# Optimization experiments

Measured on AMD Instinct MI355X. Metric: run time of the kernel, lower is better.

Reference implementation:

```python
import jax, jax.numpy as jnp
import numpy as np

B, NQ, NK, D = 64, 1024, 1024, 128
MASK_VALUE = -1e6


def setup_inputs() -> dict:
    key = jax.random.key(0)
    kq, kk, kv, kl = jax.random.split(key, 4)
    queries = jax.random.normal(kq, (B, NQ, D), dtype=jnp.float32)
    keys = jax.random.normal(kk, (B, NK, D), dtype=jnp.float32)
    values = jax.random.normal(kv, (B, NK, D), dtype=jnp.float32)
    valid_lens = jax.random.randint(kl, (B,), 1, NK + 1, dtype=jnp.int32)
    return {"queries": queries, "keys": keys, "values": values, "valid_lens": valid_lens}


def reference(queries, keys, values, valid_lens):
    d = queries.shape[-1]
    # scores: [B, Nq, Nk]
    scores = jnp.einsum("bqd,bkd->bqk", queries, keys) / jnp.sqrt(jnp.float32(d))
    # valid_lens [B] -> mask over last (key) axis, same for every query row
    key_pos = jnp.arange(scores.shape[-1])  # [Nk]
    mask = key_pos[None, None, :] < valid_lens[:, None, None]  # [B,1,Nk] broadcast
    scores = jnp.where(mask, scores, jnp.float32(MASK_VALUE))
    attn = jax.nn.softmax(scores, axis=-1)
    # dropout p=0.0 (eval): identity
    return jnp.einsum("bqk,bkd->bqd", attn, values)
```

## Files before the change

kernel.cpp:

```cpp
#include <hip/hip_runtime.h>

typedef __bf16 bf16x8 __attribute__((ext_vector_type(8)));
typedef __bf16 bf16x2 __attribute__((ext_vector_type(2)));
typedef float f32x4 __attribute__((ext_vector_type(4)));
typedef float f32x16 __attribute__((ext_vector_type(16)));
typedef int i32x4 __attribute__((ext_vector_type(4)));

namespace {
constexpr int kNQ = 1024;
constexpr int kNK = 1024;
constexpr int kD = 128;
constexpr int kBK = 32;
constexpr int kTileElems = 4096;
constexpr float kScaleLog2e = 0.12751742f;
}

__device__ __forceinline__ int packbf(float a, float b) {
    bf16x2 t; t[0] = (__bf16)a; t[1] = (__bf16)b;
    return __builtin_bit_cast(int, t);
}

__global__ void repack(const float* __restrict__ K, const float* __restrict__ V,
                       const int* __restrict__ VL,
                       __bf16* __restrict__ Kimg, __bf16* __restrict__ Vimg,
                       int* __restrict__ perm) {
    const int blk = blockIdx.x;

    if (blk == 64 * 32) {
        const int t = threadIdx.x;
        if (t < 64) {
            const int v = VL[t];
            int rank = 0;
            for (int j = 0; j < 64; ++j) {
                const int vj = VL[j];
                rank += (vj > v) || (vj == v && j < t);
            }
            perm[rank] = t;
        }
        return;
    }

    const int b = blk >> 5, t = blk & 31;
    if (t * kBK >= VL[b]) return;
    const int tid = threadIdx.x;
    __shared__ float vbuf[32 * 132];

    const size_t tileofs = (size_t)(b * 32 + t) * kTileElems;

    {
        const int key = tid >> 3, s = tid & 7;
        const float* src = K + (((size_t)b * kNK + t * kBK + key) * kD + s * 16);
        const f32x4 x0 = *(const f32x4*)(src + 0);
        const f32x4 x1 = *(const f32x4*)(src + 4);
        const f32x4 x2 = *(const f32x4*)(src + 8);
        const f32x4 x3 = *(const f32x4*)(src + 12);
        bf16x8 h0, h1;
        #pragma unroll
        for (int j = 0; j < 4; ++j) {
            h0[j] = (__bf16)x0[j]; h0[4 + j] = (__bf16)x1[j];
            h1[j] = (__bf16)x2[j]; h1[4 + j] = (__bf16)x3[j];
        }
        *(bf16x8*)(Kimg + tileofs + (s * 64 + key) * 8)      = h0;
        *(bf16x8*)(Kimg + tileofs + (s * 64 + 32 + key) * 8) = h1;
    }

    {
        const int r = tid >> 3, col0 = (tid & 7) * 16;
        const float* src = V + (((size_t)b * kNK + t * kBK + r) * kD + col0);
        #pragma unroll
        for (int j = 0; j < 4; ++j) {
            const f32x4 x = *(const f32x4*)(src + j * 4);
            *(f32x4*)&vbuf[r * 132 + col0 + j * 4] = x;
        }
    }
    __syncthreads();
    #pragma unroll
    for (int it = 0; it < 2; ++it) {
        const int ch  = tid + it * 256;
        const int db  = ch >> 7;
        const int s   = (ch >> 6) & 1;
        const int hi  = (ch >> 5) & 1;
        const int key = ch & 31;
        const int d   = db * 32 + key;
        const int k8  = s * 16 + hi * 8;
        bf16x8 h;
        #pragma unroll
        for (int j = 0; j < 8; ++j) h[j] = (__bf16)vbuf[(k8 + j) * 132 + d];
        *(bf16x8*)(Vimg + tileofs + ch * 8) = h;
    }
}

__global__ __launch_bounds__(256, 2)
void fa_fwd(const float* __restrict__ Q, const int* __restrict__ VL,
            const int* __restrict__ perm, const __bf16* __restrict__ Kimg,
            const __bf16* __restrict__ Vimg, float* __restrict__ O)
{
    const int tid  = threadIdx.x;
    const int wave = tid >> 6;
    const int lane = tid & 63;
    const int key  = lane & 31;
    const int hi   = lane >> 5;

    const int i = blockIdx.x;
    const int j = i & 255;
    const int rank = (i >> 8) ? (511 - j) : j;

    const int b  = perm[rank >> 3];
    const int q0 = (rank & 7) * 128 + wave * 32;

    const int valid  = VL[b];
    const int ntiles = (valid + kBK - 1) / kBK;
    const __bf16* kbase = Kimg + (size_t)b * 32 * kTileElems;
    const __bf16* vbase = Vimg + (size_t)b * 32 * kTileElems;
    const int fofs = lane * 8;

    bf16x8 qf[8];
    {
        const float* qp = Q + ((size_t)b * kNQ + q0 + key) * kD + hi * 8;
        #pragma unroll
        for (int s = 0; s < 8; ++s) {
            const f32x4 x0 = *(const f32x4*)(qp + s * 16);
            const f32x4 x1 = *(const f32x4*)(qp + s * 16 + 4);
            #pragma unroll
            for (int jj = 0; jj < 4; ++jj) {
                qf[s][jj]     = (__bf16)x0[jj];
                qf[s][4 + jj] = (__bf16)x1[jj];
            }
        }
    }

    bf16x8 kr[8], vr[8];
    #pragma unroll
    for (int s = 0; s < 8; ++s)
        kr[s] = *(const bf16x8*)(kbase + s * 512 + fofs);
    #pragma unroll
    for (int f = 0; f < 8; ++f)
        vr[f] = *(const bf16x8*)(vbase + f * 512 + fofs);

    f32x16 acc0, acc1, acc2, acc3;
    #pragma unroll
    for (int r = 0; r < 16; ++r) { acc0[r]=0.f; acc1[r]=0.f; acc2[r]=0.f; acc3[r]=0.f; }
    float lsum = 0.f;

    const int xaddr = (lane ^ 32) << 2;
    const int hi4   = hi << 2;

    for (int t = 0; t < ntiles; ++t) {
        f32x16 sa, sb;
        #pragma unroll
        for (int r = 0; r < 16; ++r) { sa[r] = 0.f; sb[r] = 0.f; }
        __builtin_amdgcn_s_setprio(1);
        #pragma unroll
        for (int s = 0; s < 4; ++s)
            sa = __builtin_amdgcn_mfma_f32_32x32x16_bf16(kr[s], qf[s], sa, 0, 0, 0);
        #pragma unroll
        for (int s = 4; s < 8; ++s)
            sb = __builtin_amdgcn_mfma_f32_32x32x16_bf16(kr[s], qf[s], sb, 0, 0, 0);
        __builtin_amdgcn_s_setprio(0);

        if (t + 1 < ntiles) {
            const __bf16* kt = kbase + (size_t)(t + 1) * kTileElems;
            #pragma unroll
            for (int s = 0; s < 8; ++s)
                kr[s] = *(const bf16x8*)(kt + s * 512 + fofs);
        }

        f32x16 sv = sa + sb;

        const int kb = t * kBK;
        if (kb + kBK > valid) {
            #pragma unroll
            for (int r = 0; r < 16; ++r) {
                const int cr = (r & 3) + 8 * (r >> 2);
                if (kb + cr + hi4 >= valid) sv[r] = -1e30f;
            }
        }

        #pragma unroll
        for (int r = 0; r < 16; ++r) sv[r] = __builtin_amdgcn_exp2f(sv[r] * kScaleLog2e);

        {
            float a0 = sv[0]+sv[1], a1 = sv[2]+sv[3], a2 = sv[4]+sv[5], a3 = sv[6]+sv[7];
            float a4 = sv[8]+sv[9], a5 = sv[10]+sv[11], a6 = sv[12]+sv[13], a7 = sv[14]+sv[15];
            lsum += ((a0+a1)+(a2+a3)) + ((a4+a5)+(a6+a7));
        }

        int w[8], pw[8];
        #pragma unroll
        for (int jp = 0; jp < 8; ++jp) w[jp] = packbf(sv[2*jp], sv[2*jp+1]);
        #pragma unroll
        for (int jp = 0; jp < 8; ++jp) pw[jp] = __builtin_amdgcn_ds_bpermute(xaddr, w[jp]);

        i32x4 f0, f1;
        f0[0] = hi ? pw[2] : w[0];
        f0[1] = hi ? pw[3] : w[1];
        f0[2] = hi ? w[2]  : pw[0];
        f0[3] = hi ? w[3]  : pw[1];
        f1[0] = hi ? pw[6] : w[4];
        f1[1] = hi ? pw[7] : w[5];
        f1[2] = hi ? w[6]  : pw[4];
        f1[3] = hi ? w[7]  : pw[5];
        const bf16x8 pfs0 = __builtin_bit_cast(bf16x8, f0);
        const bf16x8 pfs1 = __builtin_bit_cast(bf16x8, f1);

        __builtin_amdgcn_s_setprio(1);
        acc0 = __builtin_amdgcn_mfma_f32_32x32x16_bf16(pfs0, vr[0], acc0, 0, 0, 0);
        acc1 = __builtin_amdgcn_mfma_f32_32x32x16_bf16(pfs0, vr[2], acc1, 0, 0, 0);
        acc2 = __builtin_amdgcn_mfma_f32_32x32x16_bf16(pfs0, vr[4], acc2, 0, 0, 0);
        acc3 = __builtin_amdgcn_mfma_f32_32x32x16_bf16(pfs0, vr[6], acc3, 0, 0, 0);
        acc0 = __builtin_amdgcn_mfma_f32_32x32x16_bf16(pfs1, vr[1], acc0, 0, 0, 0);
        acc1 = __builtin_amdgcn_mfma_f32_32x32x16_bf16(pfs1, vr[3], acc1, 0, 0, 0);
        acc2 = __builtin_amdgcn_mfma_f32_32x32x16_bf16(pfs1, vr[5], acc2, 0, 0, 0);
        acc3 = __builtin_amdgcn_mfma_f32_32x32x16_bf16(pfs1, vr[7], acc3, 0, 0, 0);
        __builtin_amdgcn_s_setprio(0);

        if (t + 1 < ntiles) {
            const __bf16* vt = vbase + (size_t)(t + 1) * kTileElems;
            #pragma unroll
            for (int f = 0; f < 8; ++f)
                vr[f] = *(const bf16x8*)(vt + f * 512 + fofs);
        }
    }

    const int plb = __builtin_amdgcn_ds_bpermute(xaddr, __builtin_bit_cast(int, lsum));
    const float linv = 1.0f / (lsum + __builtin_bit_cast(float, plb));
    float* ob = O + ((size_t)b * kNQ + q0) * kD;
    const int hib = hi << 4;
    #pragma unroll
    for (int r = 0; r < 16; ++r) {
        const int cr = (r & 3) + 8 * (r >> 2);
        const int iv = __builtin_amdgcn_ds_bpermute((cr << 2) + hib,
                                                    __builtin_bit_cast(int, linv));
        const float inv = __builtin_bit_cast(float, iv);
        const int q = cr + hi4;
        ob[q * kD +   0 + key] = acc0[r] * inv;
        ob[q * kD +  32 + key] = acc1[r] * inv;
        ob[q * kD +  64 + key] = acc2[r] * inv;
        ob[q * kD +  96 + key] = acc3[r] * inv;
    }
}

extern "C" void kernel_launch(void* const* d_in, const int* in_sizes, int n_in,
                              void* d_out, int out_size, void* d_ws, size_t ws_size,
                              hipStream_t stream) {
    const float* Q = (const float*)d_in[0];
    const float* K = (const float*)d_in[1];
    const float* V = (const float*)d_in[2];
    const int*  VL = (const int*)d_in[3];
    float* O = (float*)d_out;

    int* perm = (int*)d_ws;
    __bf16* Kimg = (__bf16*)((char*)d_ws + 4096);
    __bf16* Vimg = (__bf16*)((char*)d_ws + 4096 + (size_t)16 * 1024 * 1024);

    repack<<<dim3(64 * 32 + 1), 256, 0, stream>>>(K, V, VL, Kimg, Vimg, perm);
    fa_fwd<<<dim3(512), 256, 0, stream>>>(Q, VL, perm, Kimg, Vimg, O);
}
```

Baseline: 163.5 us.

## Split key range across two blocks and add combine kernel

Each query chunk is now processed by two blocks that each cover half of the key tiles, doubling the grid. Partial unnormalized outputs and row sums are written to global memory, and a new combine kernel adds the halves and divides by the total sum. This aims to increase parallelism and balance per-block work, at the cost of extra global traffic for the partial outputs and an additional kernel launch.

```diff
diff --git a/kernel.cpp b/kernel.cpp
--- a/kernel.cpp
+++ b/kernel.cpp
@@ -10,6 +10,7 @@
 constexpr int kNQ = 1024;
 constexpr int kNK = 1024;
 constexpr int kD = 128;
+constexpr int kB  = 64;
 constexpr int kBK = 32;
 constexpr int kTileElems = 4096;
 constexpr float kScaleLog2e = 0.12751742f;
@@ -93,7 +94,8 @@
 __global__ __launch_bounds__(256, 2)
 void fa_fwd(const float* __restrict__ Q, const int* __restrict__ VL,
             const int* __restrict__ perm, const __bf16* __restrict__ Kimg,
-            const __bf16* __restrict__ Vimg, float* __restrict__ O)
+            const __bf16* __restrict__ Vimg, float* __restrict__ Onum,
+            float* __restrict__ Npart, float* __restrict__ Lpart)
 {
     const int tid  = threadIdx.x;
     const int wave = tid >> 6;
@@ -102,14 +104,21 @@
     const int hi   = lane >> 5;
 
     const int i = blockIdx.x;
-    const int j = i & 255;
-    const int rank = (i >> 8) ? (511 - j) : j;
-
-    const int b  = perm[rank >> 3];
-    const int q0 = (rank & 7) * 128 + wave * 32;
+    const int j = i & 511;
+    const int rank = (i >> 9) ? (1023 - j) : j;
+
+    const int b    = perm[rank >> 4];
+    const int sub  = rank & 15;
+    const int qc   = sub >> 1;
+    const int kpar = sub & 1;
+    const int q0   = qc * 128 + wave * 32;
 
     const int valid  = VL[b];
     const int ntiles = (valid + kBK - 1) / kBK;
+    const int nt0    = (ntiles + 1) >> 1;
+    const int tbeg   = kpar ? nt0 : 0;
+    const int tend   = kpar ? ntiles : nt0;
+
     const __bf16* kbase = Kimg + (size_t)b * 32 * kTileElems;
     const __bf16* vbase = Vimg + (size_t)b * 32 * kTileElems;
     const int fofs = lane * 8;
@@ -130,12 +139,14 @@
     }
 
     bf16x8 kr[8], vr[8];
-    #pragma unroll
-    for (int s = 0; s < 8; ++s)
-        kr[s] = *(const bf16x8*)(kbase + s * 512 + fofs);
-    #pragma unroll
-    for (int f = 0; f < 8; ++f)
-        vr[f] = *(const bf16x8*)(vbase + f * 512 + fofs);
+    {
+        const __bf16* kt0 = kbase + (size_t)tbeg * kTileElems;
+        const __bf16* vt0 = vbase + (size_t)tbeg * kTileElems;
+        #pragma unroll
+        for (int s = 0; s < 8; ++s) kr[s] = *(const bf16x8*)(kt0 + s * 512 + fofs);
+        #pragma unroll
+        for (int f = 0; f < 8; ++f) vr[f] = *(const bf16x8*)(vt0 + f * 512 + fofs);
+    }
 
     f32x16 acc0, acc1, acc2, acc3;
     #pragma unroll
@@ -145,7 +156,7 @@
     const int xaddr = (lane ^ 32) << 2;
     const int hi4   = hi << 2;
 
-    for (int t = 0; t < ntiles; ++t) {
+    for (int t = tbeg; t < tend; ++t) {
         f32x16 sa, sb;
         #pragma unroll
         for (int r = 0; r < 16; ++r) { sa[r] = 0.f; sb[r] = 0.f; }
@@ -158,11 +169,10 @@
             sb = __builtin_amdgcn_mfma_f32_32x32x16_bf16(kr[s], qf[s], sb, 0, 0, 0);
         __builtin_amdgcn_s_setprio(0);
 
-        if (t + 1 < ntiles) {
+        if (t + 1 < tend) {
             const __bf16* kt = kbase + (size_t)(t + 1) * kTileElems;
             #pragma unroll
-            for (int s = 0; s < 8; ++s)
-                kr[s] = *(const bf16x8*)(kt + s * 512 + fofs);
+            for (int s = 0; s < 8; ++s) kr[s] = *(const bf16x8*)(kt + s * 512 + fofs);
         }
 
         f32x16 sv = sa + sb;
@@ -214,29 +224,45 @@
         acc3 = __builtin_amdgcn_mfma_f32_32x32x16_bf16(pfs1, vr[7], acc3, 0, 0, 0);
         __builtin_amdgcn_s_setprio(0);
 
-        if (t + 1 < ntiles) {
+        if (t + 1 < tend) {
             const __bf16* vt = vbase + (size_t)(t + 1) * kTileElems;
             #pragma unroll
-            for (int f = 0; f < 8; ++f)
-                vr[f] = *(const bf16x8*)(vt + f * 512 + fofs);
+            for (int f = 0; f < 8; ++f) vr[f] = *(const bf16x8*)(vt + f * 512 + fofs);
         }
     }
 
     const int plb = __builtin_amdgcn_ds_bpermute(xaddr, __builtin_bit_cast(int, lsum));
-    const float linv = 1.0f / (lsum + __builtin_bit_cast(float, plb));
-    float* ob = O + ((size_t)b * kNQ + q0) * kD;
-    const int hib = hi << 4;
+    const float lrow = lsum + __builtin_bit_cast(float, plb);
+    if (hi == 0) Lpart[((size_t)kpar * kB + b) * kNQ + q0 + key] = lrow;
+
+    float* nb = (kpar ? Npart : Onum) + ((size_t)b * kNQ + q0) * kD;
     #pragma unroll
     for (int r = 0; r < 16; ++r) {
         const int cr = (r & 3) + 8 * (r >> 2);
-        const int iv = __builtin_amdgcn_ds_bpermute((cr << 2) + hib,
-                                                    __builtin_bit_cast(int, linv));
-        const float inv = __builtin_bit_cast(float, iv);
         const int q = cr + hi4;
-        ob[q * kD +   0 + key] = acc0[r] * inv;
-        ob[q * kD +  32 + key] = acc1[r] * inv;
-        ob[q * kD +  64 + key] = acc2[r] * inv;
-        ob[q * kD +  96 + key] = acc3[r] * inv;
+        nb[q * kD +   0 + key] = acc0[r];
+        nb[q * kD +  32 + key] = acc1[r];
+        nb[q * kD +  64 + key] = acc2[r];
+        nb[q * kD +  96 + key] = acc3[r];
+    }
+}
+
+__global__ __launch_bounds__(256)
+void combine(float* __restrict__ O, const float* __restrict__ Npart,
+             const float* __restrict__ Lpart)
+{
+    const size_t idx = (size_t)blockIdx.x * 256 + threadIdx.x;
+    #pragma unroll
+    for (int u = 0; u < 4; ++u) {
+        const size_t c = idx * 4 + u;
+        const size_t row = c >> 5;
+        const float l = Lpart[row] + Lpart[(size_t)kB * kNQ + row];
+        const float inv = 1.0f / l;
+        f32x4 n0 = *((const f32x4*)O + c);
+        const f32x4 n1 = *((const f32x4*)Npart + c);
+        #pragma unroll
+        for (int e = 0; e < 4; ++e) n0[e] = (n0[e] + n1[e]) * inv;
+        *((f32x4*)O + c) = n0;
     }
 }
 
@@ -249,10 +275,14 @@
     const int*  VL = (const int*)d_in[3];
     float* O = (float*)d_out;
 
-    int* perm = (int*)d_ws;
+    int* perm    = (int*)d_ws;
     __bf16* Kimg = (__bf16*)((char*)d_ws + 4096);
     __bf16* Vimg = (__bf16*)((char*)d_ws + 4096 + (size_t)16 * 1024 * 1024);
+    float* Npart = (float*)((char*)d_ws + 4096 + (size_t)32 * 1024 * 1024);
+    float* Lpart = (float*)((char*)d_ws + 4096 + (size_t)32 * 1024 * 1024
+                            + (size_t)kB * kNQ * kD * sizeof(float));
 
     repack<<<dim3(64 * 32 + 1), 256, 0, stream>>>(K, V, VL, Kimg, Vimg, perm);
-    fa_fwd<<<dim3(512), 256, 0, stream>>>(Q, VL, perm, Kimg, Vimg, O);
-}
+    fa_fwd<<<dim3(1024), 256, 0, stream>>>(Q, VL, perm, Kimg, Vimg, O, Npart, Lpart);
+    combine<<<dim3(2048), 256, 0, stream>>>(O, Npart, Lpart);
+}
```

Result: slower. 191.4 us (+17.0%).

## Fuse K/V bf16 repack into attention kernel via double-buffered LDS staging

Applied to the files above, without the earlier changes.

Removes the separate repack kernel and its workspace round-trip. Each block now loads fp32 K/V tiles from global memory, converts them to bf16 in the MFMA fragment layout, and stages them in double-buffered LDS, prefetching the next tile while computing the current one. The batch ordering by valid length is computed in-wave with ds_bpermute instead of a separate perm array. The cost is that each of the 8 blocks per batch now re-reads and re-converts the fp32 K/V, V is read with strided scalar loads, and every tile adds block barriers and LDS traffic.

```diff
diff --git a/kernel.cpp b/kernel.cpp
--- a/kernel.cpp
+++ b/kernel.cpp
@@ -20,81 +20,14 @@
     return __builtin_bit_cast(int, t);
 }
 
-__global__ void repack(const float* __restrict__ K, const float* __restrict__ V,
-                       const int* __restrict__ VL,
-                       __bf16* __restrict__ Kimg, __bf16* __restrict__ Vimg,
-                       int* __restrict__ perm) {
-    const int blk = blockIdx.x;
-
-    if (blk == 64 * 32) {
-        const int t = threadIdx.x;
-        if (t < 64) {
-            const int v = VL[t];
-            int rank = 0;
-            for (int j = 0; j < 64; ++j) {
-                const int vj = VL[j];
-                rank += (vj > v) || (vj == v && j < t);
-            }
-            perm[rank] = t;
-        }
-        return;
-    }
-
-    const int b = blk >> 5, t = blk & 31;
-    if (t * kBK >= VL[b]) return;
-    const int tid = threadIdx.x;
-    __shared__ float vbuf[32 * 132];
-
-    const size_t tileofs = (size_t)(b * 32 + t) * kTileElems;
-
-    {
-        const int key = tid >> 3, s = tid & 7;
-        const float* src = K + (((size_t)b * kNK + t * kBK + key) * kD + s * 16);
-        const f32x4 x0 = *(const f32x4*)(src + 0);
-        const f32x4 x1 = *(const f32x4*)(src + 4);
-        const f32x4 x2 = *(const f32x4*)(src + 8);
-        const f32x4 x3 = *(const f32x4*)(src + 12);
-        bf16x8 h0, h1;
-        #pragma unroll
-        for (int j = 0; j < 4; ++j) {
-            h0[j] = (__bf16)x0[j]; h0[4 + j] = (__bf16)x1[j];
-            h1[j] = (__bf16)x2[j]; h1[4 + j] = (__bf16)x3[j];
-        }
-        *(bf16x8*)(Kimg + tileofs + (s * 64 + key) * 8)      = h0;
-        *(bf16x8*)(Kimg + tileofs + (s * 64 + 32 + key) * 8) = h1;
-    }
-
-    {
-        const int r = tid >> 3, col0 = (tid & 7) * 16;
-        const float* src = V + (((size_t)b * kNK + t * kBK + r) * kD + col0);
-        #pragma unroll
-        for (int j = 0; j < 4; ++j) {
-            const f32x4 x = *(const f32x4*)(src + j * 4);
-            *(f32x4*)&vbuf[r * 132 + col0 + j * 4] = x;
-        }
-    }
-    __syncthreads();
-    #pragma unroll
-    for (int it = 0; it < 2; ++it) {
-        const int ch  = tid + it * 256;
-        const int db  = ch >> 7;
-        const int s   = (ch >> 6) & 1;
-        const int hi  = (ch >> 5) & 1;
-        const int key = ch & 31;
-        const int d   = db * 32 + key;
-        const int k8  = s * 16 + hi * 8;
-        bf16x8 h;
-        #pragma unroll
-        for (int j = 0; j < 8; ++j) h[j] = (__bf16)vbuf[(k8 + j) * 132 + d];
-        *(bf16x8*)(Vimg + tileofs + ch * 8) = h;
-    }
-}
-
 __global__ __launch_bounds__(256, 2)
-void fa_fwd(const float* __restrict__ Q, const int* __restrict__ VL,
-            const int* __restrict__ perm, const __bf16* __restrict__ Kimg,
-            const __bf16* __restrict__ Vimg, float* __restrict__ O)
+void fa_fused(const float* __restrict__ Q, const float* __restrict__ K,
+              const float* __restrict__ V, const int* __restrict__ VL,
+              float* __restrict__ O)
 {
+    __shared__ __align__(16) __bf16 kls[2][kTileElems];
+    __shared__ __align__(16) __bf16 vls[2][kTileElems];
+
     const int tid  = threadIdx.x;
     const int wave = tid >> 6;
     const int lane = tid & 63;
@@ -102,17 +35,78 @@
     const int hi   = lane >> 5;
 
     const int i = blockIdx.x;
-    const int j = i & 255;
-    const int rank = (i >> 8) ? (511 - j) : j;
-
-    const int b  = perm[rank >> 3];
+    const int jj_ = i & 255;
+    const int rank = (i >> 8) ? (511 - jj_) : jj_;
+    int b;
+    {
+        const int myv = VL[lane];
+        int rk = 0;
+        #pragma unroll
+        for (int j = 0; j < 64; ++j) {
+            const int vj = __builtin_amdgcn_ds_bpermute(j << 2, myv);
+            rk += (vj > myv) || (vj == myv && j < lane);
+        }
+        const int inv = __builtin_amdgcn_ds_permute(rk << 2, lane);
+        b = __builtin_amdgcn_ds_bpermute((rank >> 3) << 2, inv);
+    }
     const int q0 = (rank & 7) * 128 + wave * 32;
 
     const int valid  = VL[b];
     const int ntiles = (valid + kBK - 1) / kBK;
-    const __bf16* kbase = Kimg + (size_t)b * 32 * kTileElems;
-    const __bf16* vbase = Vimg + (size_t)b * 32 * kTileElems;
-    const int fofs = lane * 8;
+    const float* Kb = K + (size_t)b * kNK * kD;
+    const float* Vb = V + (size_t)b * kNK * kD;
+
+    const int cha = tid, chb = tid + 256;
+    const int ka_off = (cha & 31) * kD + ((cha >> 6) * 16 + ((cha >> 5) & 1) * 8);
+    const int kb_off = (chb & 31) * kD + ((chb >> 6) * 16 + ((chb >> 5) & 1) * 8);
+    const int va_row = ((cha >> 6) & 1) * 16 + ((cha >> 5) & 1) * 8;
+    const int va_col = (cha >> 7) * 32 + (cha & 31);
+    const int vb_row = ((chb >> 6) & 1) * 16 + ((chb >> 5) & 1) * 8;
+    const int vb_col = (chb >> 7) * 32 + (chb & 31);
+
+    float kraw[16];
+    float vraw[16];
+
+    auto stage_issue = [&](int t) {
+        const float* Kt = Kb + (size_t)t * kBK * kD;
+        const float* Vt = Vb + (size_t)t * kBK * kD;
+        {
+            const f32x4 x0 = *(const f32x4*)(Kt + ka_off);
+            const f32x4 x1 = *(const f32x4*)(Kt + ka_off + 4);
+            const f32x4 x2 = *(const f32x4*)(Kt + kb_off);
+            const f32x4 x3 = *(const f32x4*)(Kt + kb_off + 4);
+            #pragma unroll
+            for (int e = 0; e < 4; ++e) {
+                kraw[e] = x0[e]; kraw[4 + e] = x1[e];
+                kraw[8 + e] = x2[e]; kraw[12 + e] = x3[e];
+            }
+        }
+        #pragma unroll
+        for (int j = 0; j < 8; ++j)
+            vraw[j] = Vt[(va_row + j) * kD + va_col];
+        #pragma unroll
+        for (int j = 0; j < 8; ++j)
+            vraw[8 + j] = Vt[(vb_row + j) * kD + vb_col];
+    };
+
+    auto stage_write = [&](int bufi) {
+        bf16x8 h;
+        #pragma unroll
+        for (int e = 0; e < 8; ++e) h[e] = (__bf16)kraw[e];
+        *(bf16x8*)&kls[bufi][cha * 8] = h;
+        #pragma unroll
+        for (int e = 0; e < 8; ++e) h[e] = (__bf16)kraw[8 + e];
+        *(bf16x8*)&kls[bufi][chb * 8] = h;
+        i32x4 p;
+        p[0] = packbf(vraw[0], vraw[1]); p[1] = packbf(vraw[2], vraw[3]);
+        p[2] = packbf(vraw[4], vraw[5]); p[3] = packbf(vraw[6], vraw[7]);
+        *(i32x4*)&vls[bufi][cha * 8] = p;
+        p[0] = packbf(vraw[8], vraw[9]);  p[1] = packbf(vraw[10], vraw[11]);
+        p[2] = packbf(vraw[12], vraw[13]); p[3] = packbf(vraw[14], vraw[15]);
+        *(i32x4*)&vls[bufi][chb * 8] = p;
+    };
+
+    stage_issue(0);
 
     bf16x8 qf[8];
     {
@@ -122,20 +116,15 @@
             const f32x4 x0 = *(const f32x4*)(qp + s * 16);
             const f32x4 x1 = *(const f32x4*)(qp + s * 16 + 4);
             #pragma unroll
-            for (int jj = 0; jj < 4; ++jj) {
-                qf[s][jj]     = (__bf16)x0[jj];
-                qf[s][4 + jj] = (__bf16)x1[jj];
+            for (int e = 0; e < 4; ++e) {
+                qf[s][e]     = (__bf16)x0[e];
+                qf[s][4 + e] = (__bf16)x1[e];
             }
         }
     }
-
-    bf16x8 kr[8], vr[8];
-    #pragma unroll
-    for (int s = 0; s < 8; ++s)
-        kr[s] = *(const bf16x8*)(kbase + s * 512 + fofs);
-    #pragma unroll
-    for (int f = 0; f < 8; ++f)
-        vr[f] = *(const bf16x8*)(vbase + f * 512 + fofs);
+    asm volatile("s_waitcnt vmcnt(0)" ::: "memory");
+    stage_write(0);
+    __builtin_amdgcn_s_barrier();
 
     f32x16 acc0, acc1, acc2, acc3;
     #pragma unroll
@@ -144,27 +133,29 @@
 
     const int xaddr = (lane ^ 32) << 2;
     const int hi4   = hi << 2;
+    const int fofs  = lane * 8;
 
     for (int t = 0; t < ntiles; ++t) {
+        if (t + 1 < ntiles) stage_issue(t + 1);
+
+        const __bf16* kbuf = kls[t & 1];
+        const __bf16* vbuf = vls[t & 1];
+
         f32x16 sa, sb;
         #pragma unroll
         for (int r = 0; r < 16; ++r) { sa[r] = 0.f; sb[r] = 0.f; }
         __builtin_amdgcn_s_setprio(1);
         #pragma unroll
-        for (int s = 0; s < 4; ++s)
-            sa = __builtin_amdgcn_mfma_f32_32x32x16_bf16(kr[s], qf[s], sa, 0, 0, 0);
-        #pragma unroll
-        for (int s = 4; s < 8; ++s)
-            sb = __builtin_amdgcn_mfma_f32_32x32x16_bf16(kr[s], qf[s], sb, 0, 0, 0);
+        for (int s = 0; s < 4; ++s) {
+            const bf16x8 kf = *(const bf16x8*)&kbuf[s * 512 + fofs];
+            sa = __builtin_amdgcn_mfma_f32_32x32x16_bf16(kf, qf[s], sa, 0, 0, 0);
+        }
+        #pragma unroll
+        for (int s = 4; s < 8; ++s) {
+            const bf16x8 kf = *(const bf16x8*)&kbuf[s * 512 + fofs];
+            sb = __builtin_amdgcn_mfma_f32_32x32x16_bf16(kf, qf[s], sb, 0, 0, 0);
+        }
         __builtin_amdgcn_s_setprio(0);
-
-        if (t + 1 < ntiles) {
-            const __bf16* kt = kbase + (size_t)(t + 1) * kTileElems;
-            #pragma unroll
-            for (int s = 0; s < 8; ++s)
-                kr[s] = *(const bf16x8*)(kt + s * 512 + fofs);
-        }
-
         f32x16 sv = sa + sb;
 
         const int kb = t * kBK;
@@ -204,22 +195,31 @@
         const bf16x8 pfs1 = __builtin_bit_cast(bf16x8, f1);
 
         __builtin_amdgcn_s_setprio(1);
-        acc0 = __builtin_amdgcn_mfma_f32_32x32x16_bf16(pfs0, vr[0], acc0, 0, 0, 0);
-        acc1 = __builtin_amdgcn_mfma_f32_32x32x16_bf16(pfs0, vr[2], acc1, 0, 0, 0);
-        acc2 = __builtin_amdgcn_mfma_f32_32x32x16_bf16(pfs0, vr[4], acc2, 0, 0, 0);
-        acc3 = __builtin_amdgcn_mfma_f32_32x32x16_bf16(pfs0, vr[6], acc3, 0, 0, 0);
-        acc0 = __builtin_amdgcn_mfma_f32_32x32x16_bf16(pfs1, vr[1], acc0, 0, 0, 0);
-        acc1 = __builtin_amdgcn_mfma_f32_32x32x16_bf16(pfs1, vr[3], acc1, 0, 0, 0);
-        acc2 = __builtin_amdgcn_mfma_f32_32x32x16_bf16(pfs1, vr[5], acc2, 0, 0, 0);
-        acc3 = __builtin_amdgcn_mfma_f32_32x32x16_bf16(pfs1, vr[7], acc3, 0, 0, 0);
+        {
+            const bf16x8 v0 = *(const bf16x8*)&vbuf[0 * 512 + fofs];
+            const bf16x8 v2 = *(const bf16x8*)&vbuf[2 * 512 + fofs];
+            const bf16x8 v4 = *(const bf16x8*)&vbuf[4 * 512 + fofs];
+            const bf16x8 v6 = *(const bf16x8*)&vbuf[6 * 512 + fofs];
+            acc0 = __builtin_amdgcn_mfma_f32_32x32x16_bf16(pfs0, v0, acc0, 0, 0, 0);
+            acc1 = __builtin_amdgcn_mfma_f32_32x32x16_bf16(pfs0, v2, acc1, 0, 0, 0);
+            acc2 = __builtin_amdgcn_mfma_f32_32x32x16_bf16(pfs0, v4, acc2, 0, 0, 0);
+            acc3 = __builtin_amdgcn_mfma_f32_32x32x16_bf16(pfs0, v6, acc3, 0, 0, 0);
+            const bf16x8 v1 = *(const bf16x8*)&vbuf[1 * 512 + fofs];
+            const bf16x8 v3 = *(const bf16x8*)&vbuf[3 * 512 + fofs];
+            const bf16x8 v5 = *(const bf16x8*)&vbuf[5 * 512 + fofs];
+            const bf16x8 v7 = *(const bf16x8*)&vbuf[7 * 512 + fofs];
+            acc0 = __builtin_amdgcn_mfma_f32_32x32x16_bf16(pfs1, v1, acc0, 0, 0, 0);
+            acc1 = __builtin_amdgcn_mfma_f32_32x32x16_bf16(pfs1, v3, acc1, 0, 0, 0);
+            acc2 = __builtin_amdgcn_mfma_f32_32x32x16_bf16(pfs1, v5, acc2, 0, 0, 0);
+            acc3 = __builtin_amdgcn_mfma_f32_32x32x16_bf16(pfs1, v7, acc3, 0, 0, 0);
+        }
         __builtin_amdgcn_s_setprio(0);
 
         if (t + 1 < ntiles) {
-            const __bf16* vt = vbase + (size_t)(t + 1) * kTileElems;
-            #pragma unroll
-            for (int f = 0; f < 8; ++f)
-                vr[f] = *(const bf16x8*)(vt + f * 512 + fofs);
-        }
+            asm volatile("s_waitcnt vmcnt(0)" ::: "memory");
+            stage_write((t + 1) & 1);
+        }
+        __builtin_amdgcn_s_barrier();
     }
 
     const int plb = __builtin_amdgcn_ds_bpermute(xaddr, __builtin_bit_cast(int, lsum));
@@ -249,10 +249,5 @@
     const int*  VL = (const int*)d_in[3];
     float* O = (float*)d_out;
 
-    int* perm = (int*)d_ws;
-    __bf16* Kimg = (__bf16*)((char*)d_ws + 4096);
-    __bf16* Vimg = (__bf16*)((char*)d_ws + 4096 + (size_t)16 * 1024 * 1024);
-
-    repack<<<dim3(64 * 32 + 1), 256, 0, stream>>>(K, V, VL, Kimg, Vimg, perm);
-    fa_fwd<<<dim3(512), 256, 0, stream>>>(Q, VL, perm, Kimg, Vimg, O);
-}
+    fa_fused<<<dim3(512), 256, 0, stream>>>(Q, K, V, VL, O);
+}
```

Result: slower. 173.0 us (+5.8%).
